# Kernel tuning notes

Measured on AMD Instinct MI355X. Metric: run time of the kernel, lower is better.

Reference implementation:

```python
import jax, jax.numpy as jnp
import numpy as np

N = 50000
E = 600000
HIDDEN = 128
HEADS = 4
HEAD_DIM = HIDDEN // HEADS
NEG_SLOPE = 0.2
LN_EPS = 1e-5


def setup_inputs() -> dict:
    key = jax.random.key(0)
    ks = jax.random.split(key, 16)
    s = 1.0 / np.sqrt(HIDDEN)
    inp = {
        "h": jax.random.normal(ks[0], (N, HIDDEN), dtype=jnp.float32),
        "src": jax.random.randint(ks[1], (E,), 0, N, dtype=jnp.int32),
        "dst": jax.random.randint(ks[2], (E,), 0, N, dtype=jnp.int32),
        # GATv2 params (share_weights=False, bias=True)
        "W_src": jax.random.normal(ks[3], (HIDDEN, HIDDEN), dtype=jnp.float32) * s,
        "b_src": jnp.zeros((HIDDEN,), dtype=jnp.float32),
        "W_dst": jax.random.normal(ks[4], (HIDDEN, HIDDEN), dtype=jnp.float32) * s,
        "b_dst": jnp.zeros((HIDDEN,), dtype=jnp.float32),
        "attn": jax.random.normal(ks[5], (HEADS, HEAD_DIM), dtype=jnp.float32) * s,
        # FFN params
        "W1": jax.random.normal(ks[6], (HIDDEN, 2 * HIDDEN), dtype=jnp.float32) * s,
        "bf1": jnp.zeros((2 * HIDDEN,), dtype=jnp.float32),
        "W2": jax.random.normal(ks[7], (2 * HIDDEN, HIDDEN), dtype=jnp.float32) * (1.0 / np.sqrt(2 * HIDDEN)),
        "bf2": jnp.zeros((HIDDEN,), dtype=jnp.float32),
        # LayerNorms
        "g1": jnp.ones((HIDDEN,), dtype=jnp.float32),
        "beta1": jnp.zeros((HIDDEN,), dtype=jnp.float32),
        "g2": jnp.ones((HIDDEN,), dtype=jnp.float32),
        "beta2": jnp.zeros((HIDDEN,), dtype=jnp.float32),
    }
    return inp


def _layernorm(x, g, b):
    mu = jnp.mean(x, axis=-1, keepdims=True)
    var = jnp.mean(jnp.square(x - mu), axis=-1, keepdims=True)
    return (x - mu) * jax.lax.rsqrt(var + LN_EPS) * g + b


def reference(h, src, dst, W_src, b_src, W_dst, b_dst, attn,
              W1, bf1, W2, bf2, g1, beta1, g2, beta2):
    # --- GATv2 attention (eval mode, dropouts are identity) ---
    fs = (h @ W_src + b_src).reshape(N, HEADS, HEAD_DIM)   # [N,H,D]
    fd = (h @ W_dst + b_dst).reshape(N, HEADS, HEAD_DIM)
    e = jax.nn.leaky_relu(fs[src] + fd[dst], NEG_SLOPE)    # [E,H,D]
    logits = jnp.einsum('ehd,hd->eh', e, attn)             # [E,H]
    # edge softmax over incoming edges of each dst node
    m = jax.ops.segment_max(logits, dst, num_segments=N)   # [N,H]
    m = jnp.where(jnp.isfinite(m), m, 0.0)                 # guard zero-in-degree
    a = jnp.exp(logits - m[dst])                           # [E,H]
    denom = jax.ops.segment_sum(a, dst, num_segments=N)    # [N,H]
    denom = jnp.where(denom == 0.0, 1.0, denom)
    alpha = a / denom[dst]                                 # [E,H]
    msg = fs[src] * alpha[:, :, None]                      # [E,H,D]
    rst = jax.ops.segment_sum(msg, dst, num_segments=N)    # [N,H,D]
    h_attn = rst.reshape(N, HIDDEN)
    # --- residual + LN, FFN + residual + LN ---
    h1 = _layernorm(h + h_attn, g1, beta1)
    ffn = jax.nn.gelu(h1 @ W1 + bf1, approximate=False) @ W2 + bf2
    out = _layernorm(h1 + ffn, g2, beta2)
    return out
```

## Files before the change

### kernel.cpp

```cpp
#include <hip/hip_runtime.h>
#include <math.h>

#define N_NODES 50000
#define N_EDGES 600000
#define HID 128
#define FFN_HID 256
#define NEG_SLOPE 0.2f
#define LN_EPS 1e-5f
#define BKT 64
#define CSTR 16

typedef unsigned short u16;
typedef unsigned int u32;
typedef __attribute__((ext_vector_type(8))) short short8;
typedef __attribute__((ext_vector_type(4))) float floatx4;

__device__ __forceinline__ u16 f2bf(float x) {
    unsigned int u = __float_as_uint(x);
    unsigned int r = u + 0x7FFFu + ((u >> 16) & 1u);
    return (u16)(r >> 16);
}
__device__ __forceinline__ float bflo(u32 u) { return __uint_as_float(u << 16); }
__device__ __forceinline__ float bfhi(u32 u) { return __uint_as_float(u & 0xffff0000u); }
__device__ __forceinline__ u32 packbf(float lo, float hi) {
    return (u32)f2bf(lo) | ((u32)f2bf(hi) << 16);
}
__device__ __forceinline__ float bf2f(u16 v) { return __uint_as_float(((u32)v) << 16); }
__device__ __forceinline__ float gelu_fast(float v) {
    float u = 1.5957691216057308f * fmaf(0.044715f * v * v, v, v);
    return v / (1.0f + __expf(-u));
}


__global__ __launch_bounds__(256) void swizzle_prep(
    const float* __restrict__ Wsrc, const float* __restrict__ Wdst,
    const float* __restrict__ W1, const float* __restrict__ W2,
    u16* __restrict__ B1, u16* __restrict__ B2, u16* __restrict__ B3)
{
    int t = blockIdx.x * 256 + threadIdx.x;
    const float* W; u16* out; int K, Nc, noff;
    if (t < 16384)       { W = Wsrc; out = B1; K = 128; Nc = 128; noff = 0; }
    else if (t < 32768)  { W = Wdst; out = B1; K = 128; Nc = 128; noff = 128; t -= 16384; }
    else if (t < 65536)  { W = W1;   out = B2; K = 128; Nc = 256; noff = 0;   t -= 32768; }
    else if (t < 98304)  { W = W2;   out = B3; K = 256; Nc = 128; noff = 0;   t -= 65536; }
    else return;
    int n = t % Nc, k = t / Nc;
    int ng = noff + n;
    int ksteps = K >> 5;
    int frag = (ng >> 4) * ksteps + (k >> 5);
    int lane = ((k >> 3) & 3) * 16 + (ng & 15);
    int j = k & 7;
    out[((size_t)frag * 64 + lane) * 8 + j] = f2bf(W[(size_t)k * Nc + n]);
}


__global__ __launch_bounds__(256) void scatter_gemm(
    const int* __restrict__ src, const int* __restrict__ dst,
    int* __restrict__ cursor, u16* __restrict__ ebkt,
    const float* __restrict__ h, const u16* __restrict__ Bsw,
    const float* __restrict__ bsrc, const float* __restrict__ bdst,
    u16* __restrict__ fsb, u16* __restrict__ fdb)
{
    if (blockIdx.x < 2344) {
        int e = blockIdx.x * 256 + threadIdx.x;
        if (e < N_EDGES) {
            int d = dst[e];
            int slot = atomicAdd(&cursor[d * CSTR], 1);
            if (slot < BKT) ebkt[(size_t)d * BKT + slot] = (u16)src[e];
        }
        return;
    }
    int bid = blockIdx.x - 2344;
    int tid = threadIdx.x, wave = tid >> 6, lane = tid & 63;
    int lrow = lane & 15, lq = lane >> 4;
    short8 bfrag[4][4];
    #pragma unroll
    for (int nt = 0; nt < 4; nt++)
        #pragma unroll
        for (int ks = 0; ks < 4; ks++) {
            int frag = (wave * 4 + nt) * 4 + ks;
            bfrag[nt][ks] = *(const short8*)(Bsw + ((size_t)frag * 64 + lane) * 8);
        }
    float bias[4];
    #pragma unroll
    for (int nt = 0; nt < 4; nt++) {
        int cg = wave * 64 + nt * 16 + lrow;
        bias[nt] = (cg < HID) ? bsrc[cg] : bdst[cg - HID];
    }
    for (int mb = bid; mb < N_NODES / 16; mb += 1024) {
        int m0 = mb * 16;
        const float* hrow = h + (size_t)(m0 + lrow) * HID;
        floatx4 acc[4];
        #pragma unroll
        for (int nt = 0; nt < 4; nt++) acc[nt] = {0.f, 0.f, 0.f, 0.f};
        #pragma unroll
        for (int ks = 0; ks < 4; ks++) {
            float4 va = *(const float4*)(hrow + ks * 32 + lq * 8);
            float4 vb = *(const float4*)(hrow + ks * 32 + lq * 8 + 4);
            short8 a;
            a[0] = (short)f2bf(va.x); a[1] = (short)f2bf(va.y);
            a[2] = (short)f2bf(va.z); a[3] = (short)f2bf(va.w);
            a[4] = (short)f2bf(vb.x); a[5] = (short)f2bf(vb.y);
            a[6] = (short)f2bf(vb.z); a[7] = (short)f2bf(vb.w);
            #pragma unroll
            for (int nt = 0; nt < 4; nt++)
                acc[nt] = __builtin_amdgcn_mfma_f32_16x16x32_bf16(a, bfrag[nt][ks], acc[nt], 0, 0, 0);
        }
        #pragma unroll
        for (int nt = 0; nt < 4; nt++) {
            int cg = wave * 64 + nt * 16 + lrow;
            u16* outp = (cg < HID) ? fsb : fdb;
            int c = cg & (HID - 1);
            #pragma unroll
            for (int r = 0; r < 4; r++) {
                int row = m0 + lq * 4 + r;
                outp[(size_t)row * HID + c] = f2bf(acc[nt][r] + bias[nt]);
            }
        }
    }
}


__global__ __launch_bounds__(256) void aggregate_kernel(
    const u16* __restrict__ fsb, const u16* __restrict__ fdb,
    const float* __restrict__ h, const float* __restrict__ attn,
    const int* __restrict__ cursor, const u16* __restrict__ ebkt,
    const float* __restrict__ g1, const float* __restrict__ beta1,
    u16* __restrict__ h1b)
{
    int wave = threadIdx.x >> 6, lane = threadIdx.x & 63;
    int node = blockIdx.x * 4 + wave;
    if (node >= N_NODES) return;
    int grp = lane >> 4, fl = lane & 15;
    int f = fl * 8;

    uint4 ud = *(const uint4*)&fdb[(size_t)node * HID + f];
    float fdv[8] = { bflo(ud.x), bfhi(ud.x), bflo(ud.y), bfhi(ud.y),
                     bflo(ud.z), bfhi(ud.z), bflo(ud.w), bfhi(ud.w) };
    float4 aA = *(const float4*)&attn[f];
    float4 aB = *(const float4*)&attn[f + 4];
    float c1[8] = { 0.6f * aA.x, 0.6f * aA.y, 0.6f * aA.z, 0.6f * aA.w,
                    0.6f * aB.x, 0.6f * aB.y, 0.6f * aB.z, 0.6f * aB.w };
    float c2[8] = { 0.4f * aA.x, 0.4f * aA.y, 0.4f * aA.z, 0.4f * aA.w,
                    0.4f * aB.x, 0.4f * aB.y, 0.4f * aB.z, 0.4f * aB.w };

    int cnt = cursor[node * CSTR]; cnt = cnt < BKT ? cnt : BKT;
    const u16* brow = ebkt + (size_t)node * BKT;
    float acc[8] = {0.f, 0.f, 0.f, 0.f, 0.f, 0.f, 0.f, 0.f};
    float lsum = 0.f;

    auto body = [&](int e) {
        int s = (int)brow[e];
        uint4 u = *(const uint4*)&fsb[(size_t)s * HID + f];
        float x[8] = { bflo(u.x), bfhi(u.x), bflo(u.y), bfhi(u.y),
                       bflo(u.z), bfhi(u.z), bflo(u.w), bfhi(u.w) };
        float p = 0.f;
        #pragma unroll
        for (int i = 0; i < 8; i++) {
            float ei = x[i] + fdv[i];
            p = fmaf(c1[i], ei, p);
            p = fmaf(c2[i], fabsf(ei), p);
        }
        p += __shfl_xor(p, 1); p += __shfl_xor(p, 2);
        float w = __expf(p);
        lsum += w;
        #pragma unroll
        for (int i = 0; i < 8; i++) acc[i] = fmaf(w, x[i], acc[i]);
    };

    int e = grp;
    for (; e + 4 < cnt; e += 8) { body(e); body(e + 4); }
    if (e < cnt) body(e);

    #pragma unroll
    for (int i = 0; i < 8; i++) {
        acc[i] += __shfl_xor(acc[i], 16);
        acc[i] += __shfl_xor(acc[i], 32);
    }
    lsum += __shfl_xor(lsum, 16); lsum += __shfl_xor(lsum, 32);

    float inv = (lsum > 0.f) ? (1.0f / lsum) : 0.f;
    float4 h0 = *(const float4*)&h[(size_t)node * HID + f];
    float4 h1v = *(const float4*)&h[(size_t)node * HID + f + 4];
    float hx[8] = { h0.x, h0.y, h0.z, h0.w, h1v.x, h1v.y, h1v.z, h1v.w };
    float o[8], s1 = 0.f, s2 = 0.f;
    #pragma unroll
    for (int i = 0; i < 8; i++) {
        o[i] = hx[i] + acc[i] * inv;
        s1 += o[i]; s2 += o[i] * o[i];
    }
    s1 += __shfl_xor(s1, 1); s2 += __shfl_xor(s2, 1);
    s1 += __shfl_xor(s1, 2); s2 += __shfl_xor(s2, 2);
    s1 += __shfl_xor(s1, 4); s2 += __shfl_xor(s2, 4);
    s1 += __shfl_xor(s1, 8); s2 += __shfl_xor(s2, 8);
    float mu = s1 * (1.0f / HID);
    float var = s2 * (1.0f / HID) - mu * mu;
    float rs = rsqrtf(var + LN_EPS);
    if (grp == 0) {
        float4 gA = *(const float4*)&g1[f], gB = *(const float4*)&g1[f + 4];
        float4 bA = *(const float4*)&beta1[f], bB = *(const float4*)&beta1[f + 4];
        float q0 = (o[0] - mu) * rs * gA.x + bA.x, q1 = (o[1] - mu) * rs * gA.y + bA.y;
        float q2 = (o[2] - mu) * rs * gA.z + bA.z, q3 = (o[3] - mu) * rs * gA.w + bA.w;
        float q4 = (o[4] - mu) * rs * gB.x + bB.x, q5 = (o[5] - mu) * rs * gB.y + bB.y;
        float q6 = (o[6] - mu) * rs * gB.z + bB.z, q7 = (o[7] - mu) * rs * gB.w + bB.w;
        uint4 ob;
        ob.x = packbf(q0, q1); ob.y = packbf(q2, q3);
        ob.z = packbf(q4, q5); ob.w = packbf(q6, q7);
        *(uint4*)&h1b[(size_t)node * HID + f] = ob;
    }
}


#define TS_PAD 8

__global__ __launch_bounds__(256) void ffn_fused(
    const u16* __restrict__ h1b,
    const u16* __restrict__ B2sw, const u16* __restrict__ B3sw,
    const float* __restrict__ bf1, const float* __restrict__ bf2,
    const float* __restrict__ g2, const float* __restrict__ beta2,
    float* __restrict__ out)
{
    __shared__ u16 ts[16][FFN_HID + TS_PAD];
    __shared__ float xs[16][HID];
    int tid = threadIdx.x, wave = tid >> 6, lane = tid & 63;
    int lrow = lane & 15, lq = lane >> 4;

    short8 b1f[4][4];
    #pragma unroll
    for (int nt = 0; nt < 4; nt++)
        #pragma unroll
        for (int ks = 0; ks < 4; ks++) {
            int frag = (wave * 4 + nt) * 4 + ks;
            b1f[nt][ks] = *(const short8*)(B2sw + ((size_t)frag * 64 + lane) * 8);
        }
    short8 b2f[2][8];
    #pragma unroll
    for (int nt = 0; nt < 2; nt++)
        #pragma unroll
        for (int ks = 0; ks < 8; ks++) {
            int frag = (wave * 2 + nt) * 8 + ks;
            b2f[nt][ks] = *(const short8*)(B3sw + ((size_t)frag * 64 + lane) * 8);
        }
    float bias1[4];
    #pragma unroll
    for (int nt = 0; nt < 4; nt++) bias1[nt] = bf1[wave * 64 + nt * 16 + lrow];
    float bias2[2];
    #pragma unroll
    for (int nt = 0; nt < 2; nt++) bias2[nt] = bf2[wave * 32 + nt * 16 + lrow];

    for (int mb = blockIdx.x; mb < N_NODES / 16; mb += gridDim.x) {
        int m0 = mb * 16;
        floatx4 acc1[4];
        #pragma unroll
        for (int nt = 0; nt < 4; nt++) acc1[nt] = {0.f, 0.f, 0.f, 0.f};
        #pragma unroll
        for (int ks = 0; ks < 4; ks++) {
            short8 a = *(const short8*)(h1b + (size_t)(m0 + lrow) * HID + ks * 32 + lq * 8);
            #pragma unroll
            for (int nt = 0; nt < 4; nt++)
                acc1[nt] = __builtin_amdgcn_mfma_f32_16x16x32_bf16(a, b1f[nt][ks], acc1[nt], 0, 0, 0);
        }
        #pragma unroll
        for (int nt = 0; nt < 4; nt++) {
            int cg = wave * 64 + nt * 16 + lrow;
            #pragma unroll
            for (int r = 0; r < 4; r++) {
                float v = acc1[nt][r] + bias1[nt];
                ts[lq * 4 + r][cg] = f2bf(gelu_fast(v));
            }
        }
        __syncthreads();
        floatx4 acc2[2];
        #pragma unroll
        for (int nt = 0; nt < 2; nt++) acc2[nt] = {0.f, 0.f, 0.f, 0.f};
        #pragma unroll
        for (int ks = 0; ks < 8; ks++) {
            short8 a = *(const short8*)&ts[lrow][ks * 32 + lq * 8];
            #pragma unroll
            for (int nt = 0; nt < 2; nt++)
                acc2[nt] = __builtin_amdgcn_mfma_f32_16x16x32_bf16(a, b2f[nt][ks], acc2[nt], 0, 0, 0);
        }
        #pragma unroll
        for (int nt = 0; nt < 2; nt++) {
            int cg = wave * 32 + nt * 16 + lrow;
            #pragma unroll
            for (int r = 0; r < 4; r++) {
                int row = m0 + lq * 4 + r;
                float resid = bf2f(h1b[(size_t)row * HID + cg]);
                xs[lq * 4 + r][cg] = acc2[nt][r] + bias2[nt] + resid;
            }
        }
        __syncthreads();
        int row = tid >> 4, c0 = (tid & 15) * 8;
        float v[8];
        float s1 = 0.f, s2 = 0.f;
        #pragma unroll
        for (int i = 0; i < 8; i++) { v[i] = xs[row][c0 + i]; s1 += v[i]; s2 += v[i] * v[i]; }
        s1 += __shfl_xor(s1, 1); s2 += __shfl_xor(s2, 1);
        s1 += __shfl_xor(s1, 2); s2 += __shfl_xor(s2, 2);
        s1 += __shfl_xor(s1, 4); s2 += __shfl_xor(s2, 4);
        s1 += __shfl_xor(s1, 8); s2 += __shfl_xor(s2, 8);
        float mu = s1 * (1.0f / HID);
        float var = s2 * (1.0f / HID) - mu * mu;
        float rs = rsqrtf(var + LN_EPS);
        float o[8];
        #pragma unroll
        for (int i = 0; i < 8; i++) o[i] = (v[i] - mu) * rs * g2[c0 + i] + beta2[c0 + i];
        float* op = out + (size_t)(m0 + row) * HID + c0;
        *(float4*)(op)     = make_float4(o[0], o[1], o[2], o[3]);
        *(float4*)(op + 4) = make_float4(o[4], o[5], o[6], o[7]);
        __syncthreads();
    }
}


extern "C" void kernel_launch(void* const* d_in, const int* in_sizes, int n_in,
                              void* d_out, int out_size, void* d_ws, size_t ws_size,
                              hipStream_t stream)
{
    const float* h    = (const float*)d_in[0];
    const int*   src  = (const int*)d_in[1];
    const int*   dst  = (const int*)d_in[2];
    const float* Wsrc = (const float*)d_in[3];
    const float* bsrc = (const float*)d_in[4];
    const float* Wdst = (const float*)d_in[5];
    const float* bdst = (const float*)d_in[6];
    const float* attn = (const float*)d_in[7];
    const float* W1   = (const float*)d_in[8];
    const float* bf1  = (const float*)d_in[9];
    const float* W2   = (const float*)d_in[10];
    const float* bf2  = (const float*)d_in[11];
    const float* g1   = (const float*)d_in[12];
    const float* beta1= (const float*)d_in[13];
    const float* g2   = (const float*)d_in[14];
    const float* beta2= (const float*)d_in[15];
    float* out = (float*)d_out;

    u16* fsb = (u16*)d_ws;
    u16* fdb = fsb + (size_t)N_NODES * HID;
    u16* h1b = fdb + (size_t)N_NODES * HID;
    u16* B1 = h1b + (size_t)N_NODES * HID;
    u16* B2 = B1 + 32768;
    u16* B3 = B2 + 32768;
    int* cursor = (int*)(B3 + 32768);
    u16* ebkt   = (u16*)(cursor + (size_t)N_NODES * CSTR);

    hipMemsetAsync(cursor, 0, (size_t)N_NODES * CSTR * sizeof(int), stream);
    swizzle_prep<<<384, 256, 0, stream>>>(Wsrc, Wdst, W1, W2, B1, B2, B3);
    scatter_gemm<<<2344 + 1024, 256, 0, stream>>>(src, dst, cursor, ebkt,
                                                  h, B1, bsrc, bdst, fsb, fdb);
    aggregate_kernel<<<(N_NODES + 3) / 4, 256, 0, stream>>>(fsb, fdb, h, attn, cursor, ebkt, g1, beta1, h1b);
    ffn_fused<<<640, 256, 0, stream>>>(h1b, B2, B3, bf1, bf2, g2, beta2, out);
}
```

Measured before the change: 232.4 us.

## Fold cursor memset into prep kernel, interleave scatter/GEMM blocks, prefetch aggregate rows

```diff
diff --git a/kernel.cpp b/kernel.cpp
--- a/kernel.cpp
+++ b/kernel.cpp
@@ -32,12 +32,19 @@
 }
 
 
-__global__ __launch_bounds__(256) void swizzle_prep(
+__global__ __launch_bounds__(256) void prep_kernel(
     const float* __restrict__ Wsrc, const float* __restrict__ Wdst,
     const float* __restrict__ W1, const float* __restrict__ W2,
-    u16* __restrict__ B1, u16* __restrict__ B2, u16* __restrict__ B3)
-{
-    int t = blockIdx.x * 256 + threadIdx.x;
+    u16* __restrict__ B1, u16* __restrict__ B2, u16* __restrict__ B3,
+    int* __restrict__ cursor)
+{
+    int b = blockIdx.x;
+    if (b >= 384) {
+        int i = (b - 384) * 256 + threadIdx.x;
+        if (i < N_NODES * CSTR) cursor[i] = 0;
+        return;
+    }
+    int t = b * 256 + threadIdx.x;
     const float* W; u16* out; int K, Nc, noff;
     if (t < 16384)       { W = Wsrc; out = B1; K = 128; Nc = 128; noff = 0; }
     else if (t < 32768)  { W = Wdst; out = B1; K = 128; Nc = 128; noff = 128; t -= 16384; }
@@ -61,8 +68,12 @@
     const float* __restrict__ bsrc, const float* __restrict__ bdst,
     u16* __restrict__ fsb, u16* __restrict__ fdb)
 {
-    if (blockIdx.x < 2344) {
-        int e = blockIdx.x * 256 + threadIdx.x;
+    int bid = blockIdx.x;
+    bool isGemm = ((bid % 3) == 0) && (bid < 3072);
+    if (!isGemm) {
+        int g_lt = (bid + 2) / 3; g_lt = g_lt < 1024 ? g_lt : 1024;
+        int sid = bid - g_lt;
+        int e = sid * 256 + threadIdx.x;
         if (e < N_EDGES) {
             int d = dst[e];
             int slot = atomicAdd(&cursor[d * CSTR], 1);
@@ -70,7 +81,7 @@
         }
         return;
     }
-    int bid = blockIdx.x - 2344;
+    int gid = bid / 3;
     int tid = threadIdx.x, wave = tid >> 6, lane = tid & 63;
     int lrow = lane & 15, lq = lane >> 4;
     short8 bfrag[4][4];
@@ -87,7 +98,7 @@
         int cg = wave * 64 + nt * 16 + lrow;
         bias[nt] = (cg < HID) ? bsrc[cg] : bdst[cg - HID];
     }
-    for (int mb = bid; mb < N_NODES / 16; mb += 1024) {
+    for (int mb = gid; mb < N_NODES / 16; mb += 1024) {
         int m0 = mb * 16;
         const float* hrow = h + (size_t)(m0 + lrow) * HID;
         floatx4 acc[4];
@@ -149,9 +160,11 @@
     float acc[8] = {0.f, 0.f, 0.f, 0.f, 0.f, 0.f, 0.f, 0.f};
     float lsum = 0.f;
 
-    auto body = [&](int e) {
+    auto loadrow = [&](int e) -> uint4 {
         int s = (int)brow[e];
-        uint4 u = *(const uint4*)&fsb[(size_t)s * HID + f];
+        return *(const uint4*)&fsb[(size_t)s * HID + f];
+    };
+    auto compute = [&](uint4 u) {
         float x[8] = { bflo(u.x), bfhi(u.x), bflo(u.y), bfhi(u.y),
                        bflo(u.z), bfhi(u.z), bflo(u.w), bfhi(u.w) };
         float p = 0.f;
@@ -168,9 +181,22 @@
         for (int i = 0; i < 8; i++) acc[i] = fmaf(w, x[i], acc[i]);
     };
 
-    int e = grp;
-    for (; e + 4 < cnt; e += 8) { body(e); body(e + 4); }
-    if (e < cnt) body(e);
+    {
+        int e = grp;
+        uint4 bufA, bufB;
+        bool vA = (e < cnt), vB = (e + 4 < cnt);
+        if (vA) bufA = loadrow(e);
+        if (vB) bufB = loadrow(e + 4);
+        while (vA) {
+            int en = e + 8;
+            uint4 bufC; bool vC = (en < cnt);
+            if (vC) bufC = loadrow(en);
+            compute(bufA);
+            bufA = bufB; vA = vB;
+            bufB = bufC; vB = vC;
+            e += 4;
+        }
+    }
 
     #pragma unroll
     for (int i = 0; i < 8; i++) {
@@ -345,10 +371,9 @@
     int* cursor = (int*)(B3 + 32768);
     u16* ebkt   = (u16*)(cursor + (size_t)N_NODES * CSTR);
 
-    hipMemsetAsync(cursor, 0, (size_t)N_NODES * CSTR * sizeof(int), stream);
-    swizzle_prep<<<384, 256, 0, stream>>>(Wsrc, Wdst, W1, W2, B1, B2, B3);
-    scatter_gemm<<<2344 + 1024, 256, 0, stream>>>(src, dst, cursor, ebkt,
-                                                  h, B1, bsrc, bdst, fsb, fdb);
+    prep_kernel<<<384 + 3125, 256, 0, stream>>>(Wsrc, Wdst, W1, W2, B1, B2, B3, cursor);
+    scatter_gemm<<<3368, 256, 0, stream>>>(src, dst, cursor, ebkt,
+                                           h, B1, bsrc, bdst, fsb, fdb);
     aggregate_kernel<<<(N_NODES + 3) / 4, 256, 0, stream>>>(fsb, fdb, h, attn, cursor, ebkt, g1, beta1, h1b);
     ffn_fused<<<640, 256, 0, stream>>>(h1b, B2, B3, bf1, bf2, g2, beta2, out);
 }
```

Result: faster. 221.6 us (-4.7%).
